# Kernel tuning notes

Hardware: AMD Instinct MI355X
Metric: run time of the kernel (lower is better)

## Reference

```python
import jax, jax.numpy as jnp
import numpy as np

LOG2 = float(np.log(2.0))

def shifted_softplus(x):
    return jax.nn.softplus(x) - LOG2

def setup_inputs() -> dict:
    key = jax.random.key(0)
    k1, k2, k3, k4, k5, k6 = jax.random.split(key, 6)
    N, E, K, F, H = 25000, 400000, 4, 128, 128
    node_sca = jax.random.normal(k1, (N, H), dtype=jnp.float32)
    node_vec = jax.random.normal(k2, (N, K - 1, F), dtype=jnp.float32)
    edge_feats = jax.random.normal(k3, (E, K, F), dtype=jnp.float32)
    edge_index = jax.random.randint(k4, (2, E), 0, N, dtype=jnp.int64)
    # Xavier-uniform linear weights, zero biases (as in reset_parameters)
    lim1 = float(np.sqrt(6.0 / (F + H)))
    lim2 = float(np.sqrt(6.0 / (H + H)))
    W1 = jax.random.uniform(k5, (F, H), minval=-lim1, maxval=lim1, dtype=jnp.float32)
    b1 = jnp.zeros((H,), dtype=jnp.float32)
    W2 = jax.random.uniform(k6, (H, H), minval=-lim2, maxval=lim2, dtype=jnp.float32)
    b2 = jnp.zeros((H,), dtype=jnp.float32)
    return {"node_sca": node_sca, "node_vec": node_vec, "edge_feats": edge_feats,
            "edge_index": edge_index, "W1": W1, "b1": b1, "W2": W2, "b2": b2}

def reference(node_sca, node_vec, edge_feats, edge_index, W1, b1, W2, b2):
    N = node_sca.shape[0]
    i = edge_index[1]  # destination node per edge
    # scatter-sum edges -> nodes: [E,K,F] -> [N,K,F]
    agg = jax.ops.segment_sum(edge_feats, i, num_segments=N)
    agg_vec = agg[:, 1:, :]               # [N,K-1,F] vector update
    s = agg.sum(axis=1)                   # [N,F] scalar aggregate
    h = shifted_softplus(s @ W1 + b1)
    h = h @ W2 + b2                       # [N,H]
    return (node_sca + h, node_vec + agg_vec)
```

## Files before the change

### kernel.cpp

```cpp
#include <hip/hip_runtime.h>

#define LOG2F 0.69314718055994530942f
#define CAP 64

__global__ __launch_bounds__(256) void zero_detect_kernel(
        const unsigned int* __restrict__ words,
        int* __restrict__ counts, int* __restrict__ ovf_cnt,
        int* __restrict__ flag, int N) {
    const int gid = blockIdx.x * blockDim.x + threadIdx.x;
    if (gid < N) counts[gid] = 0;
    if (gid == 0) *ovf_cnt = 0;
    if (blockIdx.x == 0 && threadIdx.x < 64) {
        const int lane = threadIdx.x;
        unsigned int acc = 0;
        #pragma unroll
        for (int r = 0; r < 4; ++r) acc |= words[1 + 2 * (lane + 64 * r)];
        int any_nonzero = __any(acc != 0u);
        if (lane == 0) *flag = any_nonzero ? 0 : 1;
    }
}

__device__ __forceinline__ int load_target(const void* idx, const int* flag,
                                           int E, int e) {
    if (*flag) return (int)((const long long*)idx)[E + e];
    return ((const int*)idx)[E + e];
}

__global__ __launch_bounds__(256) void bucket_kernel(
        const void* __restrict__ idx, const int* __restrict__ flag,
        int* __restrict__ counts, int* __restrict__ elist64,
        int* __restrict__ ovf_cnt, int* __restrict__ ovf_n,
        int* __restrict__ ovf_e, int E) {
    int e = blockIdx.x * blockDim.x + threadIdx.x;
    if (e >= E) return;
    int n = load_target(idx, flag, E, e);
    int pos = atomicAdd(&counts[n], 1);
    if (pos < CAP) {
        elist64[(n << 6) + pos] = e;
    } else {
        int op = atomicAdd(ovf_cnt, 1);
        ovf_n[op] = n;
        ovf_e[op] = e;
    }
}

__global__ __launch_bounds__(256) void gather_kernel(
        const float4* __restrict__ edge_feats4,
        const int* __restrict__ elist64,
        const int* __restrict__ counts,
        const int* __restrict__ ovf_cnt,
        const int* __restrict__ ovf_n,
        const int* __restrict__ ovf_e,
        const float* __restrict__ node_vec,
        float* __restrict__ out1,
        float* __restrict__ s,
        int N) {
    const int n = blockIdx.x;
    const int tid = threadIdx.x;
    const int sub = tid >> 7;
    const int q = tid & 127;

    const int cnt = counts[n];
    const int cin = min(cnt, CAP);

    __shared__ int el[CAP];
    __shared__ float4 lds[256];

    if (tid < cin) el[tid] = elist64[(n << 6) + tid];
    __syncthreads();

    const int h0 = cin >> 1;
    const int mybase = sub ? h0 : 0;
    const int myc = sub ? (cin - h0) : h0;

    float4 acc = make_float4(0.f, 0.f, 0.f, 0.f);
    int it = 0;
    for (; it + 4 <= myc; it += 4) {
        const long long e0 = el[mybase + it + 0];
        const long long e1 = el[mybase + it + 1];
        const long long e2 = el[mybase + it + 2];
        const long long e3 = el[mybase + it + 3];
        float4 v0 = edge_feats4[e0 * 128 + q];
        float4 v1 = edge_feats4[e1 * 128 + q];
        float4 v2 = edge_feats4[e2 * 128 + q];
        float4 v3 = edge_feats4[e3 * 128 + q];
        acc.x += (v0.x + v1.x) + (v2.x + v3.x);
        acc.y += (v0.y + v1.y) + (v2.y + v3.y);
        acc.z += (v0.z + v1.z) + (v2.z + v3.z);
        acc.w += (v0.w + v1.w) + (v2.w + v3.w);
    }
    for (; it < myc; ++it) {
        const long long e = el[mybase + it];
        float4 v = edge_feats4[e * 128 + q];
        acc.x += v.x; acc.y += v.y; acc.z += v.z; acc.w += v.w;
    }

    lds[tid] = acc;
    __syncthreads();

    if (tid < 128) {
        float4 a = lds[q];
        float4 b = lds[128 + q];
        a.x += b.x; a.y += b.y; a.z += b.z; a.w += b.w;
        if (cnt > CAP) {
            int oc = *ovf_cnt;
            for (int i = 0; i < oc; ++i) {
                if (ovf_n[i] == n) {
                    float4 v = edge_feats4[(long long)ovf_e[i] * 128 + q];
                    a.x += v.x; a.y += v.y; a.z += v.z; a.w += v.w;
                }
            }
        }
        lds[q] = a;
    }
    __syncthreads();

    if (tid >= 32 && tid < 128) {
        const int o = tid - 32;
        float4 a = lds[tid];
        float4 v = ((const float4*)node_vec)[(long long)n * 96 + o];
        ((float4*)out1)[(long long)n * 96 + o] =
            make_float4(v.x + a.x, v.y + a.y, v.z + a.z, v.w + a.w);
    }
    if (tid < 32) {
        float4 a0 = lds[tid];
        float4 a1 = lds[32 + tid];
        float4 a2 = lds[64 + tid];
        float4 a3 = lds[96 + tid];
        ((float4*)s)[(long long)n * 32 + tid] =
            make_float4(a0.x + a1.x + a2.x + a3.x,
                        a0.y + a1.y + a2.y + a3.y,
                        a0.z + a1.z + a2.z + a3.z,
                        a0.w + a1.w + a2.w + a3.w);
    }
}

__global__ __launch_bounds__(256) void node_kernel(
        const float* __restrict__ s,
        const float* __restrict__ node_sca,
        const float* __restrict__ W1, const float* __restrict__ b1,
        const float* __restrict__ W2, const float* __restrict__ b2,
        float* __restrict__ out0,
        int N) {
    __shared__ float s_lds[16][128];
    __shared__ float h_lds[16][128];

    const int tid = threadIdx.x;
    const int nbase = blockIdx.x * 16;

    {
        const float4* sg = (const float4*)s;
        #pragma unroll
        for (int step = 0; step < 2; ++step) {
            int idx = tid + step * 256;
            int m = idx >> 5;
            int q = idx & 31;
            int n = nbase + m;
            float4 v = make_float4(0.f, 0.f, 0.f, 0.f);
            if (n < N) v = sg[(long long)n * 32 + q];
            *(float4*)&s_lds[m][q * 4] = v;
        }
    }
    __syncthreads();

    const int j = tid & 127;
    const int mbase = (tid >> 7) * 8;

    {
        float acc[8] = {0.f, 0.f, 0.f, 0.f, 0.f, 0.f, 0.f, 0.f};
        #pragma unroll 4
        for (int f0 = 0; f0 < 128; f0 += 4) {
            const float w0 = W1[(f0 + 0) * 128 + j];
            const float w1 = W1[(f0 + 1) * 128 + j];
            const float w2 = W1[(f0 + 2) * 128 + j];
            const float w3 = W1[(f0 + 3) * 128 + j];
            #pragma unroll
            for (int m = 0; m < 8; ++m) {
                float4 sv = *(const float4*)&s_lds[mbase + m][f0];
                acc[m] = fmaf(sv.x, w0, acc[m]);
                acc[m] = fmaf(sv.y, w1, acc[m]);
                acc[m] = fmaf(sv.z, w2, acc[m]);
                acc[m] = fmaf(sv.w, w3, acc[m]);
            }
        }
        const float bj = b1[j];
        #pragma unroll
        for (int m = 0; m < 8; ++m) {
            float x = acc[m] + bj;
            float h = fmaxf(x, 0.f) + log1pf(expf(-fabsf(x))) - LOG2F;
            h_lds[mbase + m][j] = h;
        }
    }
    __syncthreads();

    {
        float acc[8] = {0.f, 0.f, 0.f, 0.f, 0.f, 0.f, 0.f, 0.f};
        #pragma unroll 4
        for (int f0 = 0; f0 < 128; f0 += 4) {
            const float w0 = W2[(f0 + 0) * 128 + j];
            const float w1 = W2[(f0 + 1) * 128 + j];
            const float w2 = W2[(f0 + 2) * 128 + j];
            const float w3 = W2[(f0 + 3) * 128 + j];
            #pragma unroll
            for (int m = 0; m < 8; ++m) {
                float4 hv = *(const float4*)&h_lds[mbase + m][f0];
                acc[m] = fmaf(hv.x, w0, acc[m]);
                acc[m] = fmaf(hv.y, w1, acc[m]);
                acc[m] = fmaf(hv.z, w2, acc[m]);
                acc[m] = fmaf(hv.w, w3, acc[m]);
            }
        }
        const float bj = b2[j];
        #pragma unroll
        for (int m = 0; m < 8; ++m) {
            const int n = nbase + mbase + m;
            if (n < N) {
                out0[(long long)n * 128 + j] =
                    node_sca[(long long)n * 128 + j] + acc[m] + bj;
            }
        }
    }
}

extern "C" void kernel_launch(void* const* d_in, const int* in_sizes, int n_in,
                              void* d_out, int out_size, void* d_ws, size_t ws_size,
                              hipStream_t stream) {
    const float* node_sca   = (const float*)d_in[0];
    const float* node_vec   = (const float*)d_in[1];
    const float* edge_feats = (const float*)d_in[2];
    const void*  edge_index = d_in[3];
    const float* W1 = (const float*)d_in[4];
    const float* b1 = (const float*)d_in[5];
    const float* W2 = (const float*)d_in[6];
    const float* b2 = (const float*)d_in[7];

    const int H = in_sizes[5];
    const int N = in_sizes[0] / H;
    const int E = in_sizes[3] / 2;

    char* w = (char*)d_ws;
    auto take = [&](size_t bytes) {
        char* p = w;
        w += (bytes + 15) & ~(size_t)15;
        return p;
    };
    int*   counts  = (int*)take(sizeof(int) * (size_t)N);
    int*   elist64 = (int*)take(sizeof(int) * (size_t)N * CAP);
    int*   ovf_cnt = (int*)take(sizeof(int));
    int*   ovf_n   = (int*)take(sizeof(int) * (size_t)E);
    int*   ovf_e   = (int*)take(sizeof(int) * (size_t)E);
    float* s       = (float*)take(sizeof(float) * (size_t)N * 128);
    int*   flag    = (int*)take(sizeof(int));

    float* out0 = (float*)d_out;
    float* out1 = out0 + (long long)N * 128;

    zero_detect_kernel<<<(N + 255) / 256, 256, 0, stream>>>(
        (const unsigned int*)edge_index, counts, ovf_cnt, flag, N);

    bucket_kernel<<<(E + 255) / 256, 256, 0, stream>>>(
        edge_index, flag, counts, elist64, ovf_cnt, ovf_n, ovf_e, E);

    gather_kernel<<<N, 256, 0, stream>>>(
        (const float4*)edge_feats, elist64, counts, ovf_cnt, ovf_n, ovf_e,
        node_vec, out1, s, N);

    node_kernel<<<(N + 15) / 16, 256, 0, stream>>>(
        s, node_sca, W1, b1, W2, b2, out0, N);
}
```

Before: 286.4 us.

## Map one wavefront per node in gather kernel, replacing LDS with shuffles

The gather kernel now gives each node a single 64-lane wavefront, four nodes per block, where before each node had a whole 256-thread block. Edge indices stay in registers and are broadcast with __shfl, and the final K-sum uses __shfl_xor. This removes all shared memory and block-level barriers. Each lane now loads two float4s per edge, so per-thread memory-level parallelism doubles, while there are four times fewer blocks and each wave handles a whole node serially.

```diff
diff --git a/kernel.cpp b/kernel.cpp
--- a/kernel.cpp
+++ b/kernel.cpp
@@ -2,6 +2,10 @@
 
 #define LOG2F 0.69314718055994530942f
 #define CAP 64
+
+__device__ __forceinline__ float4 f4add(float4 a, float4 b) {
+    return make_float4(a.x + b.x, a.y + b.y, a.z + b.z, a.w + b.w);
+}
 
 __global__ __launch_bounds__(256) void zero_detect_kernel(
         const unsigned int* __restrict__ words,
@@ -55,83 +59,68 @@
         float* __restrict__ out1,
         float* __restrict__ s,
         int N) {
-    const int n = blockIdx.x;
-    const int tid = threadIdx.x;
-    const int sub = tid >> 7;
-    const int q = tid & 127;
+    const int wave = threadIdx.x >> 6;
+    const int lane = threadIdx.x & 63;
+    const int n = blockIdx.x * 4 + wave;
+    if (n >= N) return;
 
     const int cnt = counts[n];
-    const int cin = min(cnt, CAP);
-
-    __shared__ int el[CAP];
-    __shared__ float4 lds[256];
-
-    if (tid < cin) el[tid] = elist64[(n << 6) + tid];
-    __syncthreads();
-
-    const int h0 = cin >> 1;
-    const int mybase = sub ? h0 : 0;
-    const int myc = sub ? (cin - h0) : h0;
-
-    float4 acc = make_float4(0.f, 0.f, 0.f, 0.f);
+    const int c = min(cnt, CAP);
+
+    int el = 0;
+    if (lane < c) el = elist64[(n << 6) + lane];
+
+    float4 a0 = make_float4(0.f, 0.f, 0.f, 0.f);
+    float4 a1 = make_float4(0.f, 0.f, 0.f, 0.f);
+
     int it = 0;
-    for (; it + 4 <= myc; it += 4) {
-        const long long e0 = el[mybase + it + 0];
-        const long long e1 = el[mybase + it + 1];
-        const long long e2 = el[mybase + it + 2];
-        const long long e3 = el[mybase + it + 3];
-        float4 v0 = edge_feats4[e0 * 128 + q];
-        float4 v1 = edge_feats4[e1 * 128 + q];
-        float4 v2 = edge_feats4[e2 * 128 + q];
-        float4 v3 = edge_feats4[e3 * 128 + q];
-        acc.x += (v0.x + v1.x) + (v2.x + v3.x);
-        acc.y += (v0.y + v1.y) + (v2.y + v3.y);
-        acc.z += (v0.z + v1.z) + (v2.z + v3.z);
-        acc.w += (v0.w + v1.w) + (v2.w + v3.w);
-    }
-    for (; it < myc; ++it) {
-        const long long e = el[mybase + it];
-        float4 v = edge_feats4[e * 128 + q];
-        acc.x += v.x; acc.y += v.y; acc.z += v.z; acc.w += v.w;
-    }
-
-    lds[tid] = acc;
-    __syncthreads();
-
-    if (tid < 128) {
-        float4 a = lds[q];
-        float4 b = lds[128 + q];
-        a.x += b.x; a.y += b.y; a.z += b.z; a.w += b.w;
-        if (cnt > CAP) {
-            int oc = *ovf_cnt;
-            for (int i = 0; i < oc; ++i) {
-                if (ovf_n[i] == n) {
-                    float4 v = edge_feats4[(long long)ovf_e[i] * 128 + q];
-                    a.x += v.x; a.y += v.y; a.z += v.z; a.w += v.w;
-                }
-            }
-        }
-        lds[q] = a;
-    }
-    __syncthreads();
-
-    if (tid >= 32 && tid < 128) {
-        const int o = tid - 32;
-        float4 a = lds[tid];
-        float4 v = ((const float4*)node_vec)[(long long)n * 96 + o];
-        ((float4*)out1)[(long long)n * 96 + o] =
-            make_float4(v.x + a.x, v.y + a.y, v.z + a.z, v.w + a.w);
-    }
-    if (tid < 32) {
-        float4 a0 = lds[tid];
-        float4 a1 = lds[32 + tid];
-        float4 a2 = lds[64 + tid];
-        float4 a3 = lds[96 + tid];
-        ((float4*)s)[(long long)n * 32 + tid] =
-            make_float4(a0.x + a1.x + a2.x + a3.x,
-                        a0.y + a1.y + a2.y + a3.y,
-                        a0.z + a1.z + a2.z + a3.z,
-                        a0.w + a1.w + a2.w + a3.w);
+    for (; it + 4 <= c; it += 4) {
+        const long long e0 = __shfl(el, it + 0);
+        const long long e1 = __shfl(el, it + 1);
+        const long long e2 = __shfl(el, it + 2);
+        const long long e3 = __shfl(el, it + 3);
+        float4 v00 = edge_feats4[e0 * 128 + lane];
+        float4 v01 = edge_feats4[e0 * 128 + 64 + lane];
+        float4 v10 = edge_feats4[e1 * 128 + lane];
+        float4 v11 = edge_feats4[e1 * 128 + 64 + lane];
+        float4 v20 = edge_feats4[e2 * 128 + lane];
+        float4 v21 = edge_feats4[e2 * 128 + 64 + lane];
+        float4 v30 = edge_feats4[e3 * 128 + lane];
+        float4 v31 = edge_feats4[e3 * 128 + 64 + lane];
+        a0 = f4add(a0, f4add(f4add(v00, v10), f4add(v20, v30)));
+        a1 = f4add(a1, f4add(f4add(v01, v11), f4add(v21, v31)));
+    }
+    for (; it < c; ++it) {
+        const long long e = __shfl(el, it);
+        a0 = f4add(a0, edge_feats4[e * 128 + lane]);
+        a1 = f4add(a1, edge_feats4[e * 128 + 64 + lane]);
+    }
+    if (cnt > CAP) {
+        const int oc = *ovf_cnt;
+        for (int i = 0; i < oc; ++i) {
+            if (ovf_n[i] == n) {
+                const long long e = ovf_e[i];
+                a0 = f4add(a0, edge_feats4[e * 128 + lane]);
+                a1 = f4add(a1, edge_feats4[e * 128 + 64 + lane]);
+            }
+        }
+    }
+
+    const float4* nv = (const float4*)node_vec + (long long)n * 96;
+    float4*       o1 = (float4*)out1 + (long long)n * 96;
+    if (lane >= 32) {
+        o1[lane - 32] = f4add(nv[lane - 32], a0);
+    }
+    o1[32 + lane] = f4add(nv[32 + lane], a1);
+
+    float4 t = f4add(a0, a1);
+    float4 u;
+    u.x = __shfl_xor(t.x, 32);
+    u.y = __shfl_xor(t.y, 32);
+    u.z = __shfl_xor(t.z, 32);
+    u.w = __shfl_xor(t.w, 32);
+    if (lane < 32) {
+        ((float4*)s)[(long long)n * 32 + lane] = f4add(t, u);
     }
 }
 
@@ -261,7 +250,7 @@
     bucket_kernel<<<(E + 255) / 256, 256, 0, stream>>>(
         edge_index, flag, counts, elist64, ovf_cnt, ovf_n, ovf_e, E);
 
-    gather_kernel<<<N, 256, 0, stream>>>(
+    gather_kernel<<<(N + 3) / 4, 256, 0, stream>>>(
         (const float4*)edge_feats, elist64, counts, ovf_cnt, ovf_n, ovf_e,
         node_vec, out1, s, N);
 
```

After: 290.5 us. No clear change (+1.4%).
